# Kernel optimization log

Measured on AMD Instinct MI355X. Metric: run time of the kernel, lower is better.

The kernel has to match this reference:

```python
import jax, jax.numpy as jnp
import numpy as np

T, H, D = 32, 4096, 64  # chunk_size, n_head, head_size


def setup_inputs() -> dict:
    key = jax.random.key(0)
    ks = jax.random.split(key, 6)
    return {
        "k": jax.random.uniform(ks[0], (T, H, 1, D), dtype=jnp.float32),
        "v": jax.random.uniform(ks[1], (T, H, D, 1), dtype=jnp.float32),
        "r": jax.random.uniform(ks[2], (T, H, D, 1), dtype=jnp.float32),
        "state": jax.random.uniform(ks[3], (H, D, D), dtype=jnp.float32),
        "td": jax.random.uniform(ks[4], (T, H, D, 1), dtype=jnp.float32),
        "tf": jax.random.uniform(ks[5], (H, D, 1), dtype=jnp.float32),
    }


def reference(k, v, r, state, td, tf):
    """RWKV chunked wkv recurrence over a chunk of T steps.

    Per step t (batched over heads H):
      kv      = v_t @ k_t                 # [H,D,D] outer product (v rows, k cols)
      out_t   = (tf * kv + state) @ r_t   # [H,D,1]
      state   = kv + td_t * state         # carried head state
    Returns (out [T,H,D,1], final_state [H,D,D]).
    """

    def step(s, inp):
        k_t, v_t, r_t, td_t = inp
        kv = jnp.matmul(v_t, k_t)              # [H,D,1] @ [H,1,D] -> [H,D,D]
        out_t = jnp.matmul(tf * kv + s, r_t)   # [H,D,D] @ [H,D,1] -> [H,D,1]
        s_new = kv + td_t * s
        return s_new, out_t

    final_state, out = jax.lax.scan(step, state, (k, v, r, td))
    return out, final_state
```

## Files before the change

kernel.cpp:

```cpp
#include <hip/hip_runtime.h>


#define TT 32
#define HH 4096
#define DD 64

__global__ __launch_bounds__(64, 4)
void wkv_chunk_kernel(const float* __restrict__ k,
                      const float* __restrict__ v,
                      const float* __restrict__ r,
                      const float* __restrict__ state_in,
                      const float* __restrict__ td,
                      const float* __restrict__ tf,
                      float* __restrict__ out,
                      float* __restrict__ state_out)
{
    const int h    = blockIdx.x;
    const int lane = threadIdx.x;

    __shared__ __align__(16) float lk[DD];
    __shared__ __align__(16) float lr[DD];

    float S[DD];
    {
        const float* sp = state_in + (size_t)(h * DD + lane) * DD;
        #pragma unroll
        for (int jq = 0; jq < DD / 4; ++jq) {
            const float4 s4 = reinterpret_cast<const float4*>(sp)[jq];
            S[4 * jq + 0] = s4.x;
            S[4 * jq + 1] = s4.y;
            S[4 * jq + 2] = s4.z;
            S[4 * jq + 3] = s4.w;
        }
    }

    const float tfi = tf[h * DD + lane];

    for (int t = 0; t < TT; ++t) {
        const int base = (t * HH + h) * DD;
        const float kj  = k[base + lane];
        const float rj  = r[base + lane];
        const float vi  = v[base + lane];
        const float tdi = td[base + lane];

        lk[lane] = kj;
        lr[lane] = rj;
        __syncthreads();

        float acc = 0.0f;
        #pragma unroll
        for (int jq = 0; jq < DD / 4; ++jq) {
            const float4 k4 = reinterpret_cast<const float4*>(lk)[jq];
            const float4 r4 = reinterpret_cast<const float4*>(lr)[jq];
            float kv;
            kv = vi * k4.x;
            acc = fmaf(fmaf(tfi, kv, S[4 * jq + 0]), r4.x, acc);
            S[4 * jq + 0] = fmaf(tdi, S[4 * jq + 0], kv);
            kv = vi * k4.y;
            acc = fmaf(fmaf(tfi, kv, S[4 * jq + 1]), r4.y, acc);
            S[4 * jq + 1] = fmaf(tdi, S[4 * jq + 1], kv);
            kv = vi * k4.z;
            acc = fmaf(fmaf(tfi, kv, S[4 * jq + 2]), r4.z, acc);
            S[4 * jq + 2] = fmaf(tdi, S[4 * jq + 2], kv);
            kv = vi * k4.w;
            acc = fmaf(fmaf(tfi, kv, S[4 * jq + 3]), r4.w, acc);
            S[4 * jq + 3] = fmaf(tdi, S[4 * jq + 3], kv);
        }

        out[base + lane] = acc;
        __syncthreads();
    }

    {
        float* sp = state_out + (size_t)(h * DD + lane) * DD;
        #pragma unroll
        for (int jq = 0; jq < DD / 4; ++jq) {
            float4 s4;
            s4.x = S[4 * jq + 0];
            s4.y = S[4 * jq + 1];
            s4.z = S[4 * jq + 2];
            s4.w = S[4 * jq + 3];
            reinterpret_cast<float4*>(sp)[jq] = s4;
        }
    }
}

extern "C" void kernel_launch(void* const* d_in, const int* in_sizes, int n_in,
                              void* d_out, int out_size, void* d_ws, size_t ws_size,
                              hipStream_t stream) {
    const float* k     = (const float*)d_in[0];
    const float* v     = (const float*)d_in[1];
    const float* r     = (const float*)d_in[2];
    const float* state = (const float*)d_in[3];
    const float* td    = (const float*)d_in[4];
    const float* tf    = (const float*)d_in[5];

    float* out       = (float*)d_out;
    float* state_out = (float*)d_out + (size_t)TT * HH * DD;

    wkv_chunk_kernel<<<dim3(HH), dim3(64), 0, stream>>>(
        k, v, r, state, td, tf, out, state_out);
}
```

Baseline: 277.3 us.

## Preload all k/r into shared memory, prefetch v/td, factor tf term algebraically

Loads k and r for all T steps into shared memory once up front, removing the two barriers per time step. Prefetches v and td two steps ahead in registers, and rewrites the output as S·r plus tf*v*(k·r), with k·r computed by a wave shuffle reduction, which saves one FMA per element and splits the accumulation across four partial sums. Launch bounds drop to a minimum of 2 blocks, which allows more registers per thread at possible cost to occupancy. Floating-point summation order changes slightly.

```diff
diff --git a/kernel.cpp b/kernel.cpp
--- a/kernel.cpp
+++ b/kernel.cpp
@@ -5,7 +5,7 @@
 #define HH 4096
 #define DD 64
 
-__global__ __launch_bounds__(64, 4)
+__global__ __launch_bounds__(64, 2)
 void wkv_chunk_kernel(const float* __restrict__ k,
                       const float* __restrict__ v,
                       const float* __restrict__ r,
@@ -18,12 +18,12 @@
     const int h    = blockIdx.x;
     const int lane = threadIdx.x;
 
-    __shared__ __align__(16) float lk[DD];
-    __shared__ __align__(16) float lr[DD];
+    __shared__ __align__(16) float lk[TT][DD];
+    __shared__ __align__(16) float lr[TT][DD];
 
     float S[DD];
     {
-        const float* sp = state_in + (size_t)(h * DD + lane) * DD;
+        const float* sp = state_in + ((size_t)h * DD + lane) * DD;
         #pragma unroll
         for (int jq = 0; jq < DD / 4; ++jq) {
             const float4 s4 = reinterpret_cast<const float4*>(sp)[jq];
@@ -33,46 +33,72 @@
             S[4 * jq + 3] = s4.w;
         }
     }
-
     const float tfi = tf[h * DD + lane];
 
+    {
+        const size_t stp = (size_t)HH * DD;
+        const float* kp = k + (size_t)h * DD + lane;
+        const float* rp = r + (size_t)h * DD + lane;
+        #pragma unroll
+        for (int c = 0; c < TT / 8; ++c) {
+            float kk[8], rr[8];
+            #pragma unroll
+            for (int u = 0; u < 8; ++u) {
+                const int t = c * 8 + u;
+                kk[u] = kp[t * stp];
+                rr[u] = rp[t * stp];
+            }
+            #pragma unroll
+            for (int u = 0; u < 8; ++u) {
+                const int t = c * 8 + u;
+                lk[t][lane] = kk[u];
+                lr[t][lane] = rr[u];
+            }
+        }
+    }
+    __syncthreads();
+
+    const size_t stp = (size_t)HH * DD;
+    const float* vp = v  + (size_t)h * DD + lane;
+    const float* tp = td + (size_t)h * DD + lane;
+    float v0 = vp[0],   v1 = vp[stp];
+    float d0 = tp[0],   d1 = tp[stp];
+
     for (int t = 0; t < TT; ++t) {
-        const int base = (t * HH + h) * DD;
-        const float kj  = k[base + lane];
-        const float rj  = r[base + lane];
-        const float vi  = v[base + lane];
-        const float tdi = td[base + lane];
+        const int tpre = (t + 2 < TT) ? (t + 2) : (TT - 1);
+        const float v2 = vp[(size_t)tpre * stp];
+        const float d2 = tp[(size_t)tpre * stp];
 
-        lk[lane] = kj;
-        lr[lane] = rj;
-        __syncthreads();
+        float p = lk[t][lane] * lr[t][lane];
+        #pragma unroll
+        for (int m = 32; m >= 1; m >>= 1) p += __shfl_xor(p, m, 64);
 
-        float acc = 0.0f;
+        const float vi = v0, tdi = d0;
+
+        float a0 = 0.f, a1 = 0.f, a2 = 0.f, a3 = 0.f;
         #pragma unroll
         for (int jq = 0; jq < DD / 4; ++jq) {
-            const float4 k4 = reinterpret_cast<const float4*>(lk)[jq];
-            const float4 r4 = reinterpret_cast<const float4*>(lr)[jq];
-            float kv;
-            kv = vi * k4.x;
-            acc = fmaf(fmaf(tfi, kv, S[4 * jq + 0]), r4.x, acc);
-            S[4 * jq + 0] = fmaf(tdi, S[4 * jq + 0], kv);
-            kv = vi * k4.y;
-            acc = fmaf(fmaf(tfi, kv, S[4 * jq + 1]), r4.y, acc);
-            S[4 * jq + 1] = fmaf(tdi, S[4 * jq + 1], kv);
-            kv = vi * k4.z;
-            acc = fmaf(fmaf(tfi, kv, S[4 * jq + 2]), r4.z, acc);
-            S[4 * jq + 2] = fmaf(tdi, S[4 * jq + 2], kv);
-            kv = vi * k4.w;
-            acc = fmaf(fmaf(tfi, kv, S[4 * jq + 3]), r4.w, acc);
-            S[4 * jq + 3] = fmaf(tdi, S[4 * jq + 3], kv);
+            const float4 k4 = *reinterpret_cast<const float4*>(&lk[t][4 * jq]);
+            const float4 r4 = *reinterpret_cast<const float4*>(&lr[t][4 * jq]);
+            a0 = fmaf(S[4 * jq + 0], r4.x, a0);
+            S[4 * jq + 0] = fmaf(tdi, S[4 * jq + 0], vi * k4.x);
+            a1 = fmaf(S[4 * jq + 1], r4.y, a1);
+            S[4 * jq + 1] = fmaf(tdi, S[4 * jq + 1], vi * k4.y);
+            a2 = fmaf(S[4 * jq + 2], r4.z, a2);
+            S[4 * jq + 2] = fmaf(tdi, S[4 * jq + 2], vi * k4.z);
+            a3 = fmaf(S[4 * jq + 3], r4.w, a3);
+            S[4 * jq + 3] = fmaf(tdi, S[4 * jq + 3], vi * k4.w);
         }
 
-        out[base + lane] = acc;
-        __syncthreads();
+        out[((size_t)t * HH + h) * DD + lane] =
+            fmaf(tfi * vi, p, (a0 + a1) + (a2 + a3));
+
+        v0 = v1; v1 = v2;
+        d0 = d1; d1 = d2;
     }
 
     {
-        float* sp = state_out + (size_t)(h * DD + lane) * DD;
+        float* sp = state_out + ((size_t)h * DD + lane) * DD;
         #pragma unroll
         for (int jq = 0; jq < DD / 4; ++jq) {
             float4 s4;
```

Result: slower. 307.4 us (+10.9%).

## Pack four heads per block, drop LDS staging, prefetch v/td two steps ahead

Applied to the files above, without the earlier changes.

Each 256-thread block now handles four heads, one wavefront per head. The k and r vectors are read straight from global memory as wave-uniform float4 loads instead of being staged through shared memory behind two barriers per step. The v and td values are software-prefetched two timesteps ahead, and the dot-product accumulator is split into four partial sums to shorten the dependency chain. The intent is to remove barrier and LDS overhead and hide load latency. The cost is redundant per-lane global loads of k and r, which rely on the cache to broadcast, plus a slightly different floating-point summation order.

```diff
diff --git a/kernel.cpp b/kernel.cpp
--- a/kernel.cpp
+++ b/kernel.cpp
@@ -5,7 +5,7 @@
 #define HH 4096
 #define DD 64
 
-__global__ __launch_bounds__(64, 4)
+__global__ __launch_bounds__(256, 4)
 void wkv_chunk_kernel(const float* __restrict__ k,
                       const float* __restrict__ v,
                       const float* __restrict__ r,
@@ -15,15 +15,13 @@
                       float* __restrict__ out,
                       float* __restrict__ state_out)
 {
-    const int h    = blockIdx.x;
-    const int lane = threadIdx.x;
-
-    __shared__ __align__(16) float lk[DD];
-    __shared__ __align__(16) float lr[DD];
+    const int lane = threadIdx.x & 63;
+    const int wid  = __builtin_amdgcn_readfirstlane(threadIdx.x >> 6);
+    const int h    = blockIdx.x * 4 + wid;
 
     float S[DD];
     {
-        const float* sp = state_in + (size_t)(h * DD + lane) * DD;
+        const float* sp = state_in + ((size_t)h * DD + lane) * DD;
         #pragma unroll
         for (int jq = 0; jq < DD / 4; ++jq) {
             const float4 s4 = reinterpret_cast<const float4*>(sp)[jq];
@@ -33,46 +31,55 @@
             S[4 * jq + 3] = s4.w;
         }
     }
-
     const float tfi = tf[h * DD + lane];
 
+    const size_t stp = (size_t)HH * DD;
+    const float* vp = v  + (size_t)h * DD + lane;
+    const float* tp = td + (size_t)h * DD + lane;
+    const float* kb = k  + (size_t)h * DD;
+    const float* rb = r  + (size_t)h * DD;
+
+    float v0 = vp[0], v1 = vp[stp];
+    float d0 = tp[0], d1 = tp[stp];
+
     for (int t = 0; t < TT; ++t) {
-        const int base = (t * HH + h) * DD;
-        const float kj  = k[base + lane];
-        const float rj  = r[base + lane];
-        const float vi  = v[base + lane];
-        const float tdi = td[base + lane];
+        const int tpre = (t + 2 < TT) ? (t + 2) : (TT - 1);
+        const float v2 = vp[(size_t)tpre * stp];
+        const float d2 = tp[(size_t)tpre * stp];
 
-        lk[lane] = kj;
-        lr[lane] = rj;
-        __syncthreads();
+        const float4* kt4 = reinterpret_cast<const float4*>(kb + (size_t)t * stp);
+        const float4* rt4 = reinterpret_cast<const float4*>(rb + (size_t)t * stp);
 
-        float acc = 0.0f;
+        const float vi = v0, tdi = d0;
+        float a0 = 0.f, a1 = 0.f, a2 = 0.f, a3 = 0.f;
+
         #pragma unroll
         for (int jq = 0; jq < DD / 4; ++jq) {
-            const float4 k4 = reinterpret_cast<const float4*>(lk)[jq];
-            const float4 r4 = reinterpret_cast<const float4*>(lr)[jq];
+            const float4 k4 = kt4[jq];
+            const float4 r4 = rt4[jq];
             float kv;
             kv = vi * k4.x;
-            acc = fmaf(fmaf(tfi, kv, S[4 * jq + 0]), r4.x, acc);
+            a0 = fmaf(fmaf(tfi, kv, S[4 * jq + 0]), r4.x, a0);
             S[4 * jq + 0] = fmaf(tdi, S[4 * jq + 0], kv);
             kv = vi * k4.y;
-            acc = fmaf(fmaf(tfi, kv, S[4 * jq + 1]), r4.y, acc);
+            a1 = fmaf(fmaf(tfi, kv, S[4 * jq + 1]), r4.y, a1);
             S[4 * jq + 1] = fmaf(tdi, S[4 * jq + 1], kv);
             kv = vi * k4.z;
-            acc = fmaf(fmaf(tfi, kv, S[4 * jq + 2]), r4.z, acc);
+            a2 = fmaf(fmaf(tfi, kv, S[4 * jq + 2]), r4.z, a2);
             S[4 * jq + 2] = fmaf(tdi, S[4 * jq + 2], kv);
             kv = vi * k4.w;
-            acc = fmaf(fmaf(tfi, kv, S[4 * jq + 3]), r4.w, acc);
+            a3 = fmaf(fmaf(tfi, kv, S[4 * jq + 3]), r4.w, a3);
             S[4 * jq + 3] = fmaf(tdi, S[4 * jq + 3], kv);
         }
 
-        out[base + lane] = acc;
-        __syncthreads();
+        out[((size_t)t * HH + h) * DD + lane] = (a0 + a1) + (a2 + a3);
+
+        v0 = v1; v1 = v2;
+        d0 = d1; d1 = d2;
     }
 
     {
-        float* sp = state_out + (size_t)(h * DD + lane) * DD;
+        float* sp = state_out + ((size_t)h * DD + lane) * DD;
         #pragma unroll
         for (int jq = 0; jq < DD / 4; ++jq) {
             float4 s4;
@@ -98,6 +105,6 @@
     float* out       = (float*)d_out;
     float* state_out = (float*)d_out + (size_t)TT * HH * DD;
 
-    wkv_chunk_kernel<<<dim3(HH), dim3(64), 0, stream>>>(
+    wkv_chunk_kernel<<<dim3(HH / 4), dim3(256), 0, stream>>>(
         k, v, r, state, td, tf, out, state_out);
 }
```

Result: slower. 753.8 us (+171.9%).
